# Kernel optimization log

Measured on AMD Instinct MI355X. Metric: run time of the kernel, lower is better.

## Reference

```python
import jax, jax.numpy as jnp
import numpy as np

B = 2
SPATIAL = (480, 360, 32)  # cylindrical grid (rho, phi, z) as in Cylinder3D
N = 400000
C = 32
EPS = 1e-5
NEG_SLOPE = 0.01
OFFSETS = [(d0, d2) for d0 in (-1, 0, 1) for d2 in (-1, 0, 1)]  # kernel (3,1,3)


def setup_inputs() -> dict:
    key = jax.random.key(0)
    k1, k2 = jax.random.split(key)
    # unique active voxel coordinates: sample unique linear indices then decode
    total = B * SPATIAL[0] * SPATIAL[1] * SPATIAL[2]
    rng = np.random.default_rng(0)
    lin = rng.choice(total, size=N, replace=False).astype(np.int64)
    b = lin // (SPATIAL[0] * SPATIAL[1] * SPATIAL[2])
    r = lin % (SPATIAL[0] * SPATIAL[1] * SPATIAL[2])
    c0 = r // (SPATIAL[1] * SPATIAL[2])
    r = r % (SPATIAL[1] * SPATIAL[2])
    c1 = r // SPATIAL[2]
    c2 = r % SPATIAL[2]
    coords = jnp.asarray(np.stack([b, c0, c1, c2], axis=1), dtype=jnp.int32)
    features = jax.random.normal(k1, (N, C), dtype=jnp.float32)
    weight = jax.random.normal(k2, (9, C, C), dtype=jnp.float32) * (1.0 / np.sqrt(9 * C))
    gamma = jnp.ones((C,), dtype=jnp.float32)
    beta = jnp.zeros((C,), dtype=jnp.float32)
    return {"features": features, "coords": coords, "weight": weight,
            "gamma": gamma, "beta": beta}


def _subm_conv(features, coords, weight):
    n = features.shape[0]
    # dense coordinate -> row-index lookup table (rulebook hash)
    lookup = jnp.full((B,) + SPATIAL, -1, dtype=jnp.int32)
    lookup = lookup.at[coords[:, 0], coords[:, 1], coords[:, 2], coords[:, 3]].set(
        jnp.arange(n, dtype=jnp.int32))
    out = jnp.zeros((n, weight.shape[-1]), dtype=features.dtype)
    for k, (d0, d2) in enumerate(OFFSETS):
        n0 = coords[:, 1] + d0
        n2 = coords[:, 3] + d2
        valid = (n0 >= 0) & (n0 < SPATIAL[0]) & (n2 >= 0) & (n2 < SPATIAL[2])
        nbr = lookup[coords[:, 0],
                     jnp.clip(n0, 0, SPATIAL[0] - 1),
                     coords[:, 2],
                     jnp.clip(n2, 0, SPATIAL[2] - 1)]
        nbr = jnp.where(valid, nbr, -1)
        # gather (masked) -> GEMM -> accumulate (scatter to same active sites)
        gathered = jnp.where((nbr >= 0)[:, None],
                             features[jnp.clip(nbr, 0)], 0.0)
        out = out + gathered @ weight[k]
    return out


def reference(features, coords, weight, gamma, beta):
    x = _subm_conv(features, coords, weight)          # [N, C]
    x = jnp.where(x >= 0, x, NEG_SLOPE * x)           # LeakyReLU (before BN per forward)
    mean = jnp.mean(x, axis=0)                        # BatchNorm1d, training mode
    var = jnp.mean((x - mean) ** 2, axis=0)           # biased variance
    y = (x - mean) * jax.lax.rsqrt(var + EPS) * gamma + beta
    return y
```

## Files before the change

### kernel.cpp

```cpp
#include <hip/hip_runtime.h>
#include <hip/hip_bf16.h>

#define S0 480
#define S1 360
#define S2 32
#define CH 32
#define EPS 1e-5f
#define SLOPE 0.01f

#define LOOKUP_INTS (2 * S0 * S1 * S2)
#define LOOKUP_BYTES ((size_t)LOOKUP_INTS * 4)

typedef short short8 __attribute__((ext_vector_type(8)));
typedef float f32x16 __attribute__((ext_vector_type(16)));

__device__ __forceinline__ unsigned short f2b(float f) {
    union { __hip_bfloat16 b; unsigned short u; } v;
    v.b = __float2bfloat16(f);
    return v.u;
}

__global__ __launch_bounds__(256) void scatter_k(
    const int4* __restrict__ coords, int* __restrict__ lookup, int n)
{
    int i = blockIdx.x * 256 + threadIdx.x;
    if (i < n) {
        int4 c = coords[i];
        int lin = ((c.x * S0 + c.y) * S1 + c.z) * S2 + c.w;
        lookup[lin] = i;
    }
}

__global__ void bfrag_prep_k(const float* __restrict__ weight,
                             short8* __restrict__ bfrag)
{
    int lane = threadIdx.x;
    int half = lane >> 5;
    int col  = lane & 31;
#pragma unroll
    for (int t = 0; t < 9; ++t)
#pragma unroll
        for (int h = 0; h < 2; ++h) {
            short8 fr;
#pragma unroll
            for (int j = 0; j < 8; ++j) {
                int ic = h * 16 + half * 8 + j;
                fr[j] = (short)f2b(weight[t * (CH * CH) + ic * CH + col]);
            }
            bfrag[(t * 2 + h) * 64 + lane] = fr;
        }
}

__global__ __launch_bounds__(256) void conv_mfma_k(
    const float* __restrict__ features,
    const int4*  __restrict__ coords,
    const int*   __restrict__ lookup,
    const short8* __restrict__ bfrag,
    unsigned short* __restrict__ xout,
    float*        __restrict__ stats_part,
    int n, int ntile)
{
    int tid  = threadIdx.x;
    int lane = tid & 63;
    int wv   = tid >> 6;
    int half = lane >> 5;
    int col  = lane & 31;

    short8 B[9][2];
#pragma unroll
    for (int t = 0; t < 9; ++t) {
        B[t][0] = bfrag[(t * 2 + 0) * 64 + lane];
        B[t][1] = bfrag[(t * 2 + 1) * 64 + lane];
    }

    int tile = blockIdx.x * 4 + wv;
    bool tlive = (tile < ntile);
    int p  = tile * 32 + col;
    bool live = tlive && (p < n);
    int pc = live ? p : 0;

    int4 c = coords[pc];
    int lin = ((c.x * S0 + c.y) * S1 + c.z) * S2 + c.w;
    int nbr[9];
#pragma unroll
    for (int d0 = 0; d0 < 3; ++d0) {
        int n0 = c.y + d0 - 1;
        bool v0 = (n0 >= 0) & (n0 < S0) & live;
#pragma unroll
        for (int d2 = 0; d2 < 3; ++d2) {
            int n2 = c.w + d2 - 1;
            bool v = v0 & (n2 >= 0) & (n2 < S2);
            nbr[d0 * 3 + d2] = v ? lookup[lin + (d0 - 1) * (S1 * S2) + (d2 - 1)] : -1;
        }
    }

    short8 A0[9], A1[9];
#pragma unroll
    for (int t = 0; t < 9; ++t) {
        int nb = nbr[t];
        if (nb >= 0) {
            const float4* fp = (const float4*)(features + (size_t)nb * CH);
            float4 x0 = fp[half * 2 + 0];
            float4 x1 = fp[half * 2 + 1];
            float4 y0 = fp[half * 2 + 4];
            float4 y1 = fp[half * 2 + 5];
            short8 a0, a1;
            a0[0] = (short)f2b(x0.x); a0[1] = (short)f2b(x0.y);
            a0[2] = (short)f2b(x0.z); a0[3] = (short)f2b(x0.w);
            a0[4] = (short)f2b(x1.x); a0[5] = (short)f2b(x1.y);
            a0[6] = (short)f2b(x1.z); a0[7] = (short)f2b(x1.w);
            a1[0] = (short)f2b(y0.x); a1[1] = (short)f2b(y0.y);
            a1[2] = (short)f2b(y0.z); a1[3] = (short)f2b(y0.w);
            a1[4] = (short)f2b(y1.x); a1[5] = (short)f2b(y1.y);
            a1[6] = (short)f2b(y1.z); a1[7] = (short)f2b(y1.w);
            A0[t] = a0; A1[t] = a1;
        } else {
            short8 z;
#pragma unroll
            for (int j = 0; j < 8; ++j) z[j] = 0;
            A0[t] = z; A1[t] = z;
        }
    }

    f32x16 acc;
#pragma unroll
    for (int r = 0; r < 16; ++r) acc[r] = 0.f;
#pragma unroll
    for (int t = 0; t < 9; ++t) {
        acc = __builtin_amdgcn_mfma_f32_32x32x16_bf16(A0[t], B[t][0], acc, 0, 0, 0);
        acc = __builtin_amdgcn_mfma_f32_32x32x16_bf16(A1[t], B[t][1], acc, 0, 0, 0);
    }

    float s = 0.f, q = 0.f;
#pragma unroll
    for (int r = 0; r < 16; ++r) {
        float v = acc[r];
        v = v >= 0.f ? v : SLOPE * v;
        int row = (r & 3) + 8 * (r >> 2) + 4 * half;
        if (live) {
            xout[((size_t)tile * 32 + row) * CH + col] = f2b(v);
            s += v; q += v * v;
        }
    }

    s += __shfl_xor(s, 32);
    q += __shfl_xor(q, 32);

    __shared__ float lsum[4][32];
    __shared__ float lsq[4][32];
    if (lane < 32) { lsum[wv][col] = s; lsq[wv][col] = q; }
    __syncthreads();
    if (tid < 32) {
        stats_part[(size_t)blockIdx.x * 64 + tid] =
            lsum[0][tid] + lsum[1][tid] + lsum[2][tid] + lsum[3][tid];
    } else if (tid < 64) {
        int cc = tid - 32;
        stats_part[(size_t)blockIdx.x * 64 + tid] =
            lsq[0][cc] + lsq[1][cc] + lsq[2][cc] + lsq[3][cc];
    }
}

__global__ __launch_bounds__(256) void reduce_stats_k(
    const float* __restrict__ part, float* __restrict__ stats, int nb)
{
    int c = blockIdx.x;
    float s = 0.f;
    for (int i = threadIdx.x; i < nb; i += 256)
        s += part[(size_t)i * 64 + c];
#pragma unroll
    for (int m = 32; m > 0; m >>= 1) s += __shfl_xor(s, m, 64);
    __shared__ float red[4];
    int wv = threadIdx.x >> 6;
    if ((threadIdx.x & 63) == 0) red[wv] = s;
    __syncthreads();
    if (threadIdx.x == 0) stats[c] = red[0] + red[1] + red[2] + red[3];
}

__global__ __launch_bounds__(256) void bn_apply_k(
    const unsigned short* __restrict__ xb,
    const float* __restrict__ stats,
    const float* __restrict__ gamma,
    const float* __restrict__ beta,
    float* __restrict__ out,
    int n)
{
    int total8 = n * 4;
    int stride = gridDim.x * blockDim.x;
    int g = blockIdx.x * blockDim.x + threadIdx.x;
    int c8 = g & 3;

    float scale[8], shift[8];
    float rn = 1.0f / (float)n;
#pragma unroll
    for (int j = 0; j < 8; ++j) {
        int oc = c8 * 8 + j;
        float m  = stats[oc] * rn;
        float vv = stats[CH + oc] * rn - m * m;
        float iv = rsqrtf(vv + EPS) * gamma[oc];
        scale[j] = iv;
        shift[j] = beta[oc] - m * iv;
    }

    const short8* x8 = (const short8*)xb;
    float4* o4 = (float4*)out;
    for (; g < total8; g += stride) {
        short8 v = x8[g];
        float f[8];
#pragma unroll
        for (int j = 0; j < 8; ++j) {
            unsigned int u = ((unsigned int)(unsigned short)v[j]) << 16;
            union { unsigned int u; float f; } w; w.u = u;
            f[j] = fmaf(w.f, scale[j], shift[j]);
        }
        o4[g * 2 + 0] = make_float4(f[0], f[1], f[2], f[3]);
        o4[g * 2 + 1] = make_float4(f[4], f[5], f[6], f[7]);
    }
}

extern "C" void kernel_launch(void* const* d_in, const int* in_sizes, int n_in,
                              void* d_out, int out_size, void* d_ws, size_t ws_size,
                              hipStream_t stream)
{
    const float* features = (const float*)d_in[0];
    const int4*  coords   = (const int4*)d_in[1];
    const float* weight   = (const float*)d_in[2];
    const float* gamma    = (const float*)d_in[3];
    const float* beta     = (const float*)d_in[4];
    float* out = (float*)d_out;

    int n = in_sizes[0] / CH;
    int ntile = (n + 31) / 32;
    int conv_blocks = (ntile + 3) / 4;

    int* lookup = (int*)d_ws;
    size_t off = LOOKUP_BYTES;
    unsigned short* xout = (unsigned short*)((char*)d_ws + off);
    off += (size_t)ntile * 32 * CH * 2;
    float* stats_part = (float*)((char*)d_ws + off);
    off += (size_t)conv_blocks * 64 * sizeof(float);
    short8* bfrag = (short8*)((char*)d_ws + off);
    off += 9 * 2 * 64 * sizeof(short8);
    float* stats = (float*)((char*)d_ws + off);

    hipMemsetAsync(lookup, 0xFF, LOOKUP_BYTES, stream);

    scatter_k<<<(n + 255) / 256, 256, 0, stream>>>(coords, lookup, n);
    bfrag_prep_k<<<1, 64, 0, stream>>>(weight, bfrag);

    conv_mfma_k<<<conv_blocks, 256, 0, stream>>>(
        features, coords, lookup, bfrag, xout, stats_part, n, ntile);

    reduce_stats_k<<<64, 256, 0, stream>>>(stats_part, stats, conv_blocks);

    bn_apply_k<<<2048, 256, 0, stream>>>(xout, stats, gamma, beta, out, n);
}
```

Baseline: 98.03 us.

## Sort active voxels spatially and gather from a compact bf16 feature copy

After: 133.5 us. +36.1%, slower.

```diff
diff --git a/kernel.cpp b/kernel.cpp
--- a/kernel.cpp
+++ b/kernel.cpp
@@ -4,12 +4,15 @@
 #define S0 480
 #define S1 360
 #define S2 32
+#define SLAB (S1 * S2)
 #define CH 32
 #define EPS 1e-5f
 #define SLOPE 0.01f
 
 #define LOOKUP_INTS (2 * S0 * S1 * S2)
 #define LOOKUP_BYTES ((size_t)LOOKUP_INTS * 4)
+#define CHUNK 2048
+#define NCHUNK (LOOKUP_INTS / CHUNK)
 
 typedef short short8 __attribute__((ext_vector_type(8)));
 typedef float f32x16 __attribute__((ext_vector_type(16)));
@@ -21,13 +24,108 @@
 }
 
 __global__ __launch_bounds__(256) void scatter_k(
-    const int4* __restrict__ coords, int* __restrict__ lookup, int n)
+    const int4* __restrict__ coords, int* __restrict__ lookup,
+    int* __restrict__ ccount, int n)
 {
     int i = blockIdx.x * 256 + threadIdx.x;
     if (i < n) {
         int4 c = coords[i];
         int lin = ((c.x * S0 + c.y) * S1 + c.z) * S2 + c.w;
         lookup[lin] = i;
+        atomicAdd(&ccount[lin >> 11], 1);
+    }
+}
+
+__global__ __launch_bounds__(256) void scan_k(
+    const int* __restrict__ ccount, int* __restrict__ cbase)
+{
+    const int PER = (NCHUNK + 255) / 256;
+    int t = threadIdx.x;
+    int tsum = 0;
+    for (int j = 0; j < PER; ++j) {
+        int idx = t * PER + j;
+        if (idx < NCHUNK) tsum += ccount[idx];
+    }
+    __shared__ int sa[256], sb[256];
+    sa[t] = tsum; __syncthreads();
+    int* src = sa; int* dst = sb;
+#pragma unroll
+    for (int off = 1; off < 256; off <<= 1) {
+        dst[t] = src[t] + (t >= off ? src[t - off] : 0);
+        __syncthreads();
+        int* tmp = src; src = dst; dst = tmp;
+    }
+    int running = src[t] - tsum;
+    for (int j = 0; j < PER; ++j) {
+        int idx = t * PER + j;
+        if (idx < NCHUNK) {
+            cbase[idx] = running;
+            running += ccount[idx];
+        }
+    }
+}
+
+__global__ __launch_bounds__(256) void fill_k(
+    const float* __restrict__ features,
+    int* __restrict__ lookup,
+    const int* __restrict__ cbase,
+    int* __restrict__ orig,
+    int* __restrict__ linS,
+    unsigned short* __restrict__ featb)
+{
+    int blk = blockIdx.x;
+    int t = threadIdx.x;
+    int base_pos = blk * CHUNK + t * 8;
+
+    const int4* lp = (const int4*)(lookup + base_pos);
+    int4 v0 = lp[0], v1 = lp[1];
+    int e[8] = { v0.x, v0.y, v0.z, v0.w, v1.x, v1.y, v1.z, v1.w };
+
+    int tcnt = 0;
+#pragma unroll
+    for (int j = 0; j < 8; ++j) tcnt += (e[j] >= 0);
+
+    __shared__ int sa[256], sb[256];
+    sa[t] = tcnt; __syncthreads();
+    int* src = sa; int* dst = sb;
+#pragma unroll
+    for (int off = 1; off < 256; off <<= 1) {
+        dst[t] = src[t] + (t >= off ? src[t - off] : 0);
+        __syncthreads();
+        int* tmp = src; src = dst; dst = tmp;
+    }
+    int excl = src[t] - tcnt;
+
+    __shared__ int s_idx[CHUNK];
+    __shared__ int s_m;
+    if (t == 255) s_m = src[255];
+
+    int cb = cbase[blk];
+    int local = excl;
+#pragma unroll
+    for (int j = 0; j < 8; ++j) {
+        int idx = e[j];
+        if (idx >= 0) {
+            int pos = base_pos + j;
+            int rank = cb + local;
+            lookup[pos] = rank;
+            orig[rank] = idx;
+            linS[rank] = pos;
+            s_idx[local] = idx;
+            ++local;
+        }
+    }
+    __syncthreads();
+
+    int m = s_m;
+    ushort4* fb4 = (ushort4*)featb;
+    int j = t & 7;
+    for (int bp = t >> 3; bp < m; bp += 32) {
+        int idx = s_idx[bp];
+        float4 f = ((const float4*)(features + (size_t)idx * CH))[j];
+        ushort4 u;
+        u.x = f2b(f.x); u.y = f2b(f.y); u.z = f2b(f.z); u.w = f2b(f.w);
+        fb4[(size_t)(cb + bp) * 8 + j] = u;
     }
 }
 
@@ -51,13 +149,14 @@
         }
 }
 
-__global__ __launch_bounds__(256) void conv_mfma_k(
-    const float* __restrict__ features,
-    const int4*  __restrict__ coords,
-    const int*   __restrict__ lookup,
+__global__ __launch_bounds__(256) void conv_sorted_k(
+    const unsigned short* __restrict__ featb,
+    const int*  __restrict__ linS,
+    const int*  __restrict__ lookup,
     const short8* __restrict__ bfrag,
-    unsigned short* __restrict__ xout,
-    float*        __restrict__ stats_part,
+    const int*  __restrict__ orig,
+    float*      __restrict__ out,
+    float*      __restrict__ stats_part,
     int n, int ntile)
 {
     int tid  = threadIdx.x;
@@ -79,46 +178,40 @@
     bool live = tlive && (p < n);
     int pc = live ? p : 0;
 
-    int4 c = coords[pc];
-    int lin = ((c.x * S0 + c.y) * S1 + c.z) * S2 + c.w;
+    int lin = linS[pc];
+    int myorig = live ? orig[pc] : 0;
+    int c2 = lin & 31;
+    int c0 = (lin / SLAB) % S0;
+
     int nbr[9];
 #pragma unroll
     for (int d0 = 0; d0 < 3; ++d0) {
-        int n0 = c.y + d0 - 1;
+        int n0 = c0 + d0 - 1;
         bool v0 = (n0 >= 0) & (n0 < S0) & live;
 #pragma unroll
         for (int d2 = 0; d2 < 3; ++d2) {
-            int n2 = c.w + d2 - 1;
+            int n2 = c2 + d2 - 1;
             bool v = v0 & (n2 >= 0) & (n2 < S2);
-            nbr[d0 * 3 + d2] = v ? lookup[lin + (d0 - 1) * (S1 * S2) + (d2 - 1)] : -1;
-        }
-    }
+            nbr[d0 * 3 + d2] = v ? lookup[lin + (d0 - 1) * SLAB + (d2 - 1)] : -1;
+        }
+    }
+
+    bool act[9];
+#pragma unroll
+    for (int t = 0; t < 9; ++t) act[t] = (__any(nbr[t] >= 0) != 0);
 
     short8 A0[9], A1[9];
 #pragma unroll
     for (int t = 0; t < 9; ++t) {
+        short8 z;
+#pragma unroll
+        for (int j = 0; j < 8; ++j) z[j] = 0;
+        A0[t] = z; A1[t] = z;
         int nb = nbr[t];
         if (nb >= 0) {
-            const float4* fp = (const float4*)(features + (size_t)nb * CH);
-            float4 x0 = fp[half * 2 + 0];
-            float4 x1 = fp[half * 2 + 1];
-            float4 y0 = fp[half * 2 + 4];
-            float4 y1 = fp[half * 2 + 5];
-            short8 a0, a1;
-            a0[0] = (short)f2b(x0.x); a0[1] = (short)f2b(x0.y);
-            a0[2] = (short)f2b(x0.z); a0[3] = (short)f2b(x0.w);
-            a0[4] = (short)f2b(x1.x); a0[5] = (short)f2b(x1.y);
-            a0[6] = (short)f2b(x1.z); a0[7] = (short)f2b(x1.w);
-            a1[0] = (short)f2b(y0.x); a1[1] = (short)f2b(y0.y);
-            a1[2] = (short)f2b(y0.z); a1[3] = (short)f2b(y0.w);
-            a1[4] = (short)f2b(y1.x); a1[5] = (short)f2b(y1.y);
-            a1[6] = (short)f2b(y1.z); a1[7] = (short)f2b(y1.w);
-            A0[t] = a0; A1[t] = a1;
-        } else {
-            short8 z;
-#pragma unroll
-            for (int j = 0; j < 8; ++j) z[j] = 0;
-            A0[t] = z; A1[t] = z;
+            const short* fp = (const short*)featb + (size_t)nb * CH;
+            A0[t] = *(const short8*)(fp + half * 8);
+            A1[t] = *(const short8*)(fp + 16 + half * 8);
         }
     }
 
@@ -127,8 +220,10 @@
     for (int r = 0; r < 16; ++r) acc[r] = 0.f;
 #pragma unroll
     for (int t = 0; t < 9; ++t) {
-        acc = __builtin_amdgcn_mfma_f32_32x32x16_bf16(A0[t], B[t][0], acc, 0, 0, 0);
-        acc = __builtin_amdgcn_mfma_f32_32x32x16_bf16(A1[t], B[t][1], acc, 0, 0, 0);
+        if (act[t]) {
+            acc = __builtin_amdgcn_mfma_f32_32x32x16_bf16(A0[t], B[t][0], acc, 0, 0, 0);
+            acc = __builtin_amdgcn_mfma_f32_32x32x16_bf16(A1[t], B[t][1], acc, 0, 0, 0);
+        }
     }
 
     float s = 0.f, q = 0.f;
@@ -137,8 +232,10 @@
         float v = acc[r];
         v = v >= 0.f ? v : SLOPE * v;
         int row = (r & 3) + 8 * (r >> 2) + 4 * half;
-        if (live) {
-            xout[((size_t)tile * 32 + row) * CH + col] = f2b(v);
+        int prow = tile * 32 + row;
+        int orow = __shfl(myorig, row, 64);
+        if (tlive && prow < n) {
+            out[(size_t)orow * CH + col] = v;
             s += v; q += v * v;
         }
     }
@@ -177,23 +274,22 @@
 }
 
 __global__ __launch_bounds__(256) void bn_apply_k(
-    const unsigned short* __restrict__ xb,
+    float* __restrict__ x,
     const float* __restrict__ stats,
     const float* __restrict__ gamma,
     const float* __restrict__ beta,
-    float* __restrict__ out,
     int n)
 {
-    int total8 = n * 4;
+    int total4 = n * (CH / 4);
     int stride = gridDim.x * blockDim.x;
     int g = blockIdx.x * blockDim.x + threadIdx.x;
-    int c8 = g & 3;
-
-    float scale[8], shift[8];
+    int c4 = g & 7;
+
+    float scale[4], shift[4];
     float rn = 1.0f / (float)n;
 #pragma unroll
-    for (int j = 0; j < 8; ++j) {
-        int oc = c8 * 8 + j;
+    for (int j = 0; j < 4; ++j) {
+        int oc = c4 * 4 + j;
         float m  = stats[oc] * rn;
         float vv = stats[CH + oc] * rn - m * m;
         float iv = rsqrtf(vv + EPS) * gamma[oc];
@@ -201,19 +297,14 @@
         shift[j] = beta[oc] - m * iv;
     }
 
-    const short8* x8 = (const short8*)xb;
-    float4* o4 = (float4*)out;
-    for (; g < total8; g += stride) {
-        short8 v = x8[g];
-        float f[8];
-#pragma unroll
-        for (int j = 0; j < 8; ++j) {
-            unsigned int u = ((unsigned int)(unsigned short)v[j]) << 16;
-            union { unsigned int u; float f; } w; w.u = u;
-            f[j] = fmaf(w.f, scale[j], shift[j]);
-        }
-        o4[g * 2 + 0] = make_float4(f[0], f[1], f[2], f[3]);
-        o4[g * 2 + 1] = make_float4(f[4], f[5], f[6], f[7]);
+    float4* x4 = (float4*)x;
+    for (; g < total4; g += stride) {
+        float4 v = x4[g];
+        v.x = fmaf(v.x, scale[0], shift[0]);
+        v.y = fmaf(v.y, scale[1], shift[1]);
+        v.z = fmaf(v.z, scale[2], shift[2]);
+        v.w = fmaf(v.w, scale[3], shift[3]);
+        x4[g] = v;
     }
 }
 
@@ -232,25 +323,29 @@
     int ntile = (n + 31) / 32;
     int conv_blocks = (ntile + 3) / 4;
 
-    int* lookup = (int*)d_ws;
-    size_t off = LOOKUP_BYTES;
-    unsigned short* xout = (unsigned short*)((char*)d_ws + off);
-    off += (size_t)ntile * 32 * CH * 2;
-    float* stats_part = (float*)((char*)d_ws + off);
-    off += (size_t)conv_blocks * 64 * sizeof(float);
-    short8* bfrag = (short8*)((char*)d_ws + off);
-    off += 9 * 2 * 64 * sizeof(short8);
-    float* stats = (float*)((char*)d_ws + off);
+    char* w = (char*)d_ws;
+    int* lookup = (int*)w;                         w += LOOKUP_BYTES;
+    unsigned short* featb = (unsigned short*)w;    w += (size_t)n * CH * 2;
+    int* linS = (int*)w;                           w += (size_t)n * 4;
+    int* orig = (int*)w;                           w += (size_t)n * 4;
+    int* ccount = (int*)w;                         w += NCHUNK * 4;
+    int* cbase = (int*)w;                          w += NCHUNK * 4;
+    float* stats_part = (float*)w;                 w += (size_t)conv_blocks * 64 * 4;
+    short8* bfrag = (short8*)w;                    w += 9 * 2 * 64 * sizeof(short8);
+    float* stats = (float*)w;
 
     hipMemsetAsync(lookup, 0xFF, LOOKUP_BYTES, stream);
-
-    scatter_k<<<(n + 255) / 256, 256, 0, stream>>>(coords, lookup, n);
+    hipMemsetAsync(ccount, 0, NCHUNK * 4, stream);
+
+    scatter_k<<<(n + 255) / 256, 256, 0, stream>>>(coords, lookup, ccount, n);
     bfrag_prep_k<<<1, 64, 0, stream>>>(weight, bfrag);
-
-    conv_mfma_k<<<conv_blocks, 256, 0, stream>>>(
-        features, coords, lookup, bfrag, xout, stats_part, n, ntile);
+    scan_k<<<1, 256, 0, stream>>>(ccount, cbase);
+    fill_k<<<NCHUNK, 256, 0, stream>>>(features, lookup, cbase, orig, linS, featb);
+
+    conv_sorted_k<<<conv_blocks, 256, 0, stream>>>(
+        featb, linS, lookup, bfrag, orig, out, stats_part, n, ntile);
 
     reduce_stats_k<<<64, 256, 0, stream>>>(stats_part, stats, conv_blocks);
 
-    bn_apply_k<<<2048, 256, 0, stream>>>(xout, stats, gamma, beta, out, n);
-}
+    bn_apply_k<<<2048, 256, 0, stream>>>(out, stats, gamma, beta, n);
+}
```
